# Kernel tuning notes

Measured on AMD Instinct MI355X. Metric: run time of the kernel, lower is better.

The kernel has to match this reference:

```python
import jax, jax.numpy as jnp
import numpy as np
from jax import lax

# --- STE quantizers matching the torch autograd.Functions ---
@jax.custom_vjp
def binary_quantize_w(x):
    return jnp.sign(x)

def _bqw_fwd(x):
    return jnp.sign(x), None

def _bqw_bwd(_, g):
    return (g,)  # straight-through identity

binary_quantize_w.defvjp(_bqw_fwd, _bqw_bwd)

@jax.custom_vjp
def binary_quantize_a(x):
    return jnp.sign(x)

def _bqa_fwd(x):
    return jnp.sign(x), x

def _bqa_bwd(x, g):
    return (jnp.clip(2.0 - jnp.abs(2.0 * x), a_min=0.0) * g,)

binary_quantize_a.defvjp(_bqa_fwd, _bqa_bwd)

STRIDE = 1
PAD = 1

def setup_inputs() -> dict:
    key = jax.random.key(0)
    k1, k2, k3 = jax.random.split(key, 3)
    x = jax.random.normal(k1, (32, 256, 56, 56), dtype=jnp.float32)
    M = jax.random.normal(k2, (256, 256, 3, 3), dtype=jnp.float32)
    Alpha = jax.random.uniform(k3, (256, 1, 1), dtype=jnp.float32)
    return {"x": x, "M": M, "Alpha": Alpha}

def reference(x, M, Alpha):
    bw = binary_quantize_w(M)        # (O, I, kh, kw), +/-1
    ba = binary_quantize_a(x)        # (N, C, H, W), +/-1
    out = lax.conv_general_dilated(
        ba, bw,
        window_strides=(STRIDE, STRIDE),
        padding=[(PAD, PAD), (PAD, PAD)],
        dimension_numbers=("NCHW", "OIHW", "NCHW"),
    )
    # Alpha (O,1,1) broadcasts over (N, O, H, W) trailing dims -> per-channel scale
    return out * Alpha
```

## Files before the change

### kernel.cpp

```cpp
#include <hip/hip_runtime.h>
#include <stdint.h>


typedef __attribute__((ext_vector_type(16))) float floatx16;
typedef __attribute__((ext_vector_type(8)))  int   intx8;

#define N_IMG 32
#define C_IN  256
#define O_OUT 256
#define HP 58
#define WP 58
#define GPI 3136
#define APAD_POS ((size_t)N_IMG * HP * WP)
#define APAD_BYTES (APAD_POS * C_IN)
#define TPI 13
#define AL_GRAN 1072
#define WL_GRAN 1536
#define WPK_STEP 49152

__device__ __forceinline__ unsigned int sgn8(float x) {
    return x > 0.f ? 0x38u : (x < 0.f ? 0xB8u : 0u);
}

__device__ __forceinline__ void glds16(const unsigned char* g, unsigned char* l) {
    __builtin_amdgcn_global_load_lds(
        (const __attribute__((address_space(1))) unsigned int*)g,
        (__attribute__((address_space(3))) unsigned int*)l, 16, 0, 0);
}

__global__ __launch_bounds__(256) void binarize_act(
    const float* __restrict__ x, unsigned char* __restrict__ apad)
{
    int bid = blockIdx.x;
    int n = bid / HP;
    int hp = bid - n * HP;
    int tid = threadIdx.x;

    unsigned char* rowp = apad + ((size_t)(n * HP + hp) * WP) * C_IN;
    uint4 z = {0u, 0u, 0u, 0u};

    if (hp == 0 || hp == HP - 1) {
#pragma unroll
        for (int j = 0; j < 4; ++j) {
            int t = tid + 256 * j;
            if (t < WP * 16) {
                int w = t >> 4, g = t & 15;
                *(uint4*)(rowp + (size_t)w * C_IN + g * 16) = z;
            }
        }
        return;
    }
    int h = hp - 1;

    __shared__ unsigned int tile[C_IN * 15];
    __shared__ unsigned int lds2[56 * 65];

    const float* xb = x + ((size_t)n * C_IN) * GPI + h * 56;
#pragma unroll
    for (int j = 0; j < 14; ++j) {
        int t = tid + 256 * j;
        int ci = t / 14;
        int w4 = t - ci * 14;
        float4 v = *(const float4*)(xb + (size_t)ci * GPI + w4 * 4);
        tile[ci * 15 + w4] = sgn8(v.x) | (sgn8(v.y) << 8) |
                             (sgn8(v.z) << 16) | (sgn8(v.w) << 24);
    }
    __syncthreads();

#pragma unroll
    for (int j = 0; j < 14; ++j) {
        int t = tid + 256 * j;
        int wlo = t & 3;
        int cq  = (t >> 2) & 63;
        int whi = t >> 8;
        int sh = wlo * 8;
        unsigned int r = 0;
#pragma unroll
        for (int i = 0; i < 4; ++i) {
            unsigned int v = tile[(cq * 4 + i) * 15 + whi];
            r |= ((v >> sh) & 0xFFu) << (8 * i);
        }
        lds2[(whi * 4 + wlo) * 65 + cq] = r;
    }
    __syncthreads();

#pragma unroll
    for (int j = 0; j < 4; ++j) {
        int t = tid + 256 * j;
        if (t < 896) {
            int w = t >> 4, g = t & 15;
            uint4 v;
            v.x = lds2[w * 65 + g * 4 + 0];
            v.y = lds2[w * 65 + g * 4 + 1];
            v.z = lds2[w * 65 + g * 4 + 2];
            v.w = lds2[w * 65 + g * 4 + 3];
            *(uint4*)(rowp + (size_t)(w + 1) * C_IN + g * 16) = v;
        }
    }
    if (tid < 32) {
        int g = tid & 15;
        int col = (tid >> 4) * (WP - 1);
        *(uint4*)(rowp + (size_t)col * C_IN + g * 16) = z;
    }
}

__global__ __launch_bounds__(64) void pack_w(
    const float* __restrict__ M, unsigned char* __restrict__ wpk)
{
    int gid = blockIdx.x * 64 + threadIdx.x;
    int o = gid >> 6;
    int c4 = (gid & 63) << 2;
    int c0q = c4 >> 6;
    int c63 = c4 & 63;
    const float* mb = M + (size_t)(o * C_IN + c4) * 9;
#pragma unroll
    for (int t = 0; t < 9; ++t) {
        int kh = t / 3, kw = t - 3 * (t / 3);
        unsigned int r = sgn8(mb[t]) | (sgn8(mb[9 + t]) << 8) |
                         (sgn8(mb[18 + t]) << 16) | (sgn8(mb[27 + t]) << 24);
        size_t dst = ((size_t)(kh * 4 + c0q) * 3 + kw) * 16384 + o * 64 + c63;
        *(unsigned int*)(wpk + dst) = r;
    }
}

__global__ __launch_bounds__(256, 2) void bconv_gemm(
    const unsigned char* __restrict__ apad,
    const unsigned char* __restrict__ wpk,
    const float* __restrict__ alpha,
    float* __restrict__ out)
{
    __shared__ __align__(16) unsigned char Al[AL_GRAN * 16];
    __shared__ __align__(16) unsigned char Wl[WL_GRAN * 16];

    const int tid = threadIdx.x;
    const int wv = tid >> 6, lane = tid & 63;
    const int l31 = lane & 31, hb = lane >> 5;

    const int hw = blockIdx.x;
    const int bid = (hw & 7) * 104 + (hw >> 3);

    const int img = bid / 26;
    const int rem = bid - img * 26;
    const int tl = rem >> 1, ot = rem & 1;
    const int g0 = tl << 8;
    const int h0 = g0 / 56, w0 = g0 - h0 * 56;
    const int o_base = ot << 7;
    const int Q0 = (img * HP + h0) * WP + w0;

    int al_pos[5], al_sl[5];
#pragma unroll
    for (int it = 0; it < 5; ++it) {
        int s = (it < 4) ? (tid + (it << 8)) : (tid + 816);
        int pos = s >> 2, gI = s & 3;
        al_pos[it] = pos;
        al_sl[it]  = ((gI ^ ((pos >> 1) & 3)) << 4);
    }
    int wl_src[6];
#pragma unroll
    for (int it = 0; it < 6; ++it) {
        int s = tid + (it << 8);
        int r = s >> 2, q = s & 3;
        int kw = r >> 7, ol = r & 127;
        wl_src[it] = kw * 16384 + (o_base + ol) * 64 + ((q ^ ((r >> 1) & 3)) << 4);
    }

    const int o_half  = (wv >> 1) << 6;
    const int px_half = (wv & 1) << 7;

    int pos_tab[4], pxg[4];
#pragma unroll
    for (int nt = 0; nt < 4; ++nt) {
        int px = px_half + (nt << 5) + l31;
        pxg[nt] = g0 + px;
        int pxc = (pxg[nt] < GPI) ? px : (GPI - 1 - g0);
        pos_tab[nt] = pxc + 2 * ((w0 + pxc) / 56);
    }

    floatx16 acc[2][4] = {};

    for (int t = 0; t < 12; ++t) {
        const int kh = t >> 2, c0 = (t & 3) << 6;
        const int rowbase = Q0 + kh * WP;
        const int plim = (int)APAD_POS - 1 - rowbase;
        const unsigned char* asrc = apad + (((size_t)rowbase << 8) + c0);
        const unsigned char* wsrc = wpk + (size_t)t * WPK_STEP;

        __syncthreads();
#pragma unroll
        for (int it = 0; it < 5; ++it) {
            int p = al_pos[it] < plim ? al_pos[it] : plim;
            int dst = (it < 4) ? ((it << 8) + (wv << 6)) : (816 + (wv << 6));
            glds16(asrc + ((size_t)p << 8) + al_sl[it], &Al[(size_t)dst << 4]);
        }
#pragma unroll
        for (int it = 0; it < 6; ++it)
            glds16(wsrc + wl_src[it], &Wl[(size_t)(tid + (it << 8)) << 4]);
        __syncthreads();

#pragma unroll
        for (int kw = 0; kw < 3; ++kw) {
            union F { uint4 q[2]; intx8 v; };
            F af[2];
#pragma unroll
            for (int mt = 0; mt < 2; ++mt) {
                int rl = (kw << 7) + o_half + (mt << 5) + l31;
                int m3 = (rl >> 1) & 3;
                af[mt].q[0] = *(const uint4*)&Wl[(size_t)(rl << 6) + ((((hb << 1))     ^ m3) << 4)];
                af[mt].q[1] = *(const uint4*)&Wl[(size_t)(rl << 6) + ((((hb << 1) | 1) ^ m3) << 4)];
            }
#pragma unroll
            for (int nt = 0; nt < 4; ++nt) {
                int pos = pos_tab[nt] + kw;
                int rb = pos << 6;
                int m3 = (pos >> 1) & 3;
                F bf;
                bf.q[0] = *(const uint4*)&Al[rb + ((((hb << 1))     ^ m3) << 4)];
                bf.q[1] = *(const uint4*)&Al[rb + ((((hb << 1) | 1) ^ m3) << 4)];
#pragma unroll
                for (int mt = 0; mt < 2; ++mt)
                    acc[mt][nt] = __builtin_amdgcn_mfma_scale_f32_32x32x64_f8f6f4(
                        af[mt].v, bf.v, acc[mt][nt],
                        0, 0,
                        0, 0x7F7F7F7F,
                        0, 0x7F7F7F7F);
            }
        }
    }

#pragma unroll
    for (int mt = 0; mt < 2; ++mt) {
#pragma unroll
        for (int r = 0; r < 16; ++r) {
            int o_loc = o_half + (mt << 5) + (r & 3) + ((r >> 2) << 3) + (hb << 2);
            int o_g = o_base + o_loc;
            float a = alpha[o_g];
            float* ob = out + ((size_t)(img * O_OUT + o_g)) * GPI;
#pragma unroll
            for (int nt = 0; nt < 4; ++nt) {
                if (pxg[nt] < GPI) ob[pxg[nt]] = acc[mt][nt][r] * a;
            }
        }
    }
}

extern "C" void kernel_launch(void* const* d_in, const int* in_sizes, int n_in,
                              void* d_out, int out_size, void* d_ws, size_t ws_size,
                              hipStream_t stream) {
    const float* x     = (const float*)d_in[0];
    const float* M     = (const float*)d_in[1];
    const float* alpha = (const float*)d_in[2];
    float* out = (float*)d_out;

    unsigned char* apad = (unsigned char*)d_ws;
    unsigned char* wpk  = apad + APAD_BYTES;

    binarize_act<<<dim3(N_IMG * HP), dim3(256), 0, stream>>>(x, apad);
    pack_w<<<dim3(256), dim3(64), 0, stream>>>(M, wpk);
    bconv_gemm<<<dim3(N_IMG * TPI * 2), dim3(256), 0, stream>>>(apad, wpk, alpha, out);
}
```

Before: 263.5 us.

## Switch binary conv operands from FP8 to FP4 packing in MFMA

Activations and weights are packed as FP4 (e2m1, ±1 encoded as nibbles) instead of FP8, which halves the padded activation and packed weight buffers. The LDS tiles, the global-to-LDS load counts and the fragment reads shrink to match, and the scaled MFMA is invoked with FP4 format codes. This is meant to cut global and LDS traffic and may raise MFMA throughput, in exchange for extra nibble-packing work in the binarize kernel and a new swizzle scheme.

```diff
diff --git a/kernel.cpp b/kernel.cpp
--- a/kernel.cpp
+++ b/kernel.cpp
@@ -12,20 +12,30 @@
 #define WP 58
 #define GPI 3136
 #define APAD_POS ((size_t)N_IMG * HP * WP)
-#define APAD_BYTES (APAD_POS * C_IN)
+#define ROWB 128
+#define APAD_BYTES (APAD_POS * ROWB)
 #define TPI 13
-#define AL_GRAN 1072
-#define WL_GRAN 1536
-#define WPK_STEP 49152
-
-__device__ __forceinline__ unsigned int sgn8(float x) {
-    return x > 0.f ? 0x38u : (x < 0.f ? 0xB8u : 0u);
+#define AL_CHUNKS 536
+#define WL_CHUNKS 768
+#define WROW 8192
+#define WPK_STEP (3 * WROW)
+
+__device__ __forceinline__ unsigned int sgn4(float x) {
+    return x > 0.f ? 0x2u : (x < 0.f ? 0xAu : 0u);
 }
 
 __device__ __forceinline__ void glds16(const unsigned char* g, unsigned char* l) {
     __builtin_amdgcn_global_load_lds(
         (const __attribute__((address_space(1))) unsigned int*)g,
         (__attribute__((address_space(3))) unsigned int*)l, 16, 0, 0);
+}
+
+__device__ __forceinline__ unsigned int nib16(unsigned int w) {
+    return (w & 0xFu) | ((w >> 4) & 0xF0u) |
+           ((w >> 8) & 0xF00u) | ((w >> 12) & 0xF000u);
+}
+__device__ __forceinline__ unsigned int nibc(unsigned int lo, unsigned int hi) {
+    return nib16(lo) | (nib16(hi) << 16);
 }
 
 __global__ __launch_bounds__(256) void binarize_act(
@@ -36,16 +46,16 @@
     int hp = bid - n * HP;
     int tid = threadIdx.x;
 
-    unsigned char* rowp = apad + ((size_t)(n * HP + hp) * WP) * C_IN;
+    unsigned char* rowp = apad + (size_t)(n * HP + hp) * WP * ROWB;
     uint4 z = {0u, 0u, 0u, 0u};
 
     if (hp == 0 || hp == HP - 1) {
 #pragma unroll
-        for (int j = 0; j < 4; ++j) {
+        for (int j = 0; j < 2; ++j) {
             int t = tid + 256 * j;
-            if (t < WP * 16) {
-                int w = t >> 4, g = t & 15;
-                *(uint4*)(rowp + (size_t)w * C_IN + g * 16) = z;
+            if (t < WP * 8) {
+                int w = t >> 3, g = t & 7;
+                *(uint4*)(rowp + (size_t)w * ROWB + g * 16) = z;
             }
         }
         return;
@@ -62,8 +72,8 @@
         int ci = t / 14;
         int w4 = t - ci * 14;
         float4 v = *(const float4*)(xb + (size_t)ci * GPI + w4 * 4);
-        tile[ci * 15 + w4] = sgn8(v.x) | (sgn8(v.y) << 8) |
-                             (sgn8(v.z) << 16) | (sgn8(v.w) << 24);
+        tile[ci * 15 + w4] = sgn4(v.x) | (sgn4(v.y) << 8) |
+                             (sgn4(v.z) << 16) | (sgn4(v.w) << 24);
     }
     __syncthreads();
 
@@ -85,22 +95,24 @@
     __syncthreads();
 
 #pragma unroll
-    for (int j = 0; j < 4; ++j) {
+    for (int j = 0; j < 2; ++j) {
         int t = tid + 256 * j;
-        if (t < 896) {
-            int w = t >> 4, g = t & 15;
+        if (t < 448) {
+            int w = t >> 3, g = t & 7;
+            uint4 a = *(uint4*)&lds2[w * 65 + g * 8];
+            uint4 b = *(uint4*)&lds2[w * 65 + g * 8 + 4];
             uint4 v;
-            v.x = lds2[w * 65 + g * 4 + 0];
-            v.y = lds2[w * 65 + g * 4 + 1];
-            v.z = lds2[w * 65 + g * 4 + 2];
-            v.w = lds2[w * 65 + g * 4 + 3];
-            *(uint4*)(rowp + (size_t)(w + 1) * C_IN + g * 16) = v;
-        }
-    }
-    if (tid < 32) {
-        int g = tid & 15;
-        int col = (tid >> 4) * (WP - 1);
-        *(uint4*)(rowp + (size_t)col * C_IN + g * 16) = z;
+            v.x = nibc(a.x, a.y);
+            v.y = nibc(a.z, a.w);
+            v.z = nibc(b.x, b.y);
+            v.w = nibc(b.z, b.w);
+            *(uint4*)(rowp + (size_t)(w + 1) * ROWB + g * 16) = v;
+        }
+    }
+    if (tid < 16) {
+        int g = tid & 7;
+        int col = (tid >> 3) * (WP - 1);
+        *(uint4*)(rowp + (size_t)col * ROWB + g * 16) = z;
     }
 }
 
@@ -111,15 +123,15 @@
     int o = gid >> 6;
     int c4 = (gid & 63) << 2;
     int c0q = c4 >> 6;
-    int c63 = c4 & 63;
+    int half = (c4 & 63) >> 1;
     const float* mb = M + (size_t)(o * C_IN + c4) * 9;
 #pragma unroll
     for (int t = 0; t < 9; ++t) {
         int kh = t / 3, kw = t - 3 * (t / 3);
-        unsigned int r = sgn8(mb[t]) | (sgn8(mb[9 + t]) << 8) |
-                         (sgn8(mb[18 + t]) << 16) | (sgn8(mb[27 + t]) << 24);
-        size_t dst = ((size_t)(kh * 4 + c0q) * 3 + kw) * 16384 + o * 64 + c63;
-        *(unsigned int*)(wpk + dst) = r;
+        unsigned int r = sgn4(mb[t]) | (sgn4(mb[9 + t]) << 4) |
+                         (sgn4(mb[18 + t]) << 8) | (sgn4(mb[27 + t]) << 12);
+        size_t dst = (size_t)((kh * 4 + c0q) * 3 + kw) * WROW + o * 32 + half;
+        *(unsigned short*)(wpk + dst) = (unsigned short)r;
     }
 }
 
@@ -129,8 +141,8 @@
     const float* __restrict__ alpha,
     float* __restrict__ out)
 {
-    __shared__ __align__(16) unsigned char Al[AL_GRAN * 16];
-    __shared__ __align__(16) unsigned char Wl[WL_GRAN * 16];
+    __shared__ __align__(16) unsigned char Al[AL_CHUNKS * 16];
+    __shared__ __align__(16) unsigned char Wl[WL_CHUNKS * 16];
 
     const int tid = threadIdx.x;
     const int wv = tid >> 6, lane = tid & 63;
@@ -147,21 +159,24 @@
     const int o_base = ot << 7;
     const int Q0 = (img * HP + h0) * WP + w0;
 
-    int al_pos[5], al_sl[5];
-#pragma unroll
-    for (int it = 0; it < 5; ++it) {
-        int s = (it < 4) ? (tid + (it << 8)) : (tid + 816);
-        int pos = s >> 2, gI = s & 3;
+    int al_pos[3], al_co[3], al_dst[3], al_on[3];
+#pragma unroll
+    for (int it = 0; it < 3; ++it) {
+        int g = (it < 2) ? (tid + (it << 8)) : (512 + tid);
+        al_on[it] = (it < 2) || (tid < AL_CHUNKS - 512);
+        int pos = g >> 1;
         al_pos[it] = pos;
-        al_sl[it]  = ((gI ^ ((pos >> 1) & 3)) << 4);
-    }
-    int wl_src[6];
-#pragma unroll
-    for (int it = 0; it < 6; ++it) {
-        int s = tid + (it << 8);
-        int r = s >> 2, q = s & 3;
+        al_co[it]  = (((g & 1) ^ ((pos >> 2) & 1)) << 4);
+        al_dst[it] = g << 4;
+    }
+    int wl_src[3], wl_dst[3];
+#pragma unroll
+    for (int it = 0; it < 3; ++it) {
+        int g = tid + (it << 8);
+        int r = g >> 1, q = (g & 1) ^ ((r >> 2) & 1);
         int kw = r >> 7, ol = r & 127;
-        wl_src[it] = kw * 16384 + (o_base + ol) * 64 + ((q ^ ((r >> 1) & 3)) << 4);
+        wl_src[it] = kw * WROW + (o_base + ol) * 32 + (q << 4);
+        wl_dst[it] = g << 4;
     }
 
     const int o_half  = (wv >> 1) << 6;
@@ -177,24 +192,27 @@
     }
 
     floatx16 acc[2][4] = {};
+    const uint4 z4 = {0u, 0u, 0u, 0u};
 
     for (int t = 0; t < 12; ++t) {
-        const int kh = t >> 2, c0 = (t & 3) << 6;
+        const int kh = t >> 2;
+        const int cb0 = (t & 3) << 5;
         const int rowbase = Q0 + kh * WP;
         const int plim = (int)APAD_POS - 1 - rowbase;
-        const unsigned char* asrc = apad + (((size_t)rowbase << 8) + c0);
+        const unsigned char* asrc = apad + ((size_t)rowbase * ROWB + cb0);
         const unsigned char* wsrc = wpk + (size_t)t * WPK_STEP;
 
         __syncthreads();
 #pragma unroll
-        for (int it = 0; it < 5; ++it) {
-            int p = al_pos[it] < plim ? al_pos[it] : plim;
-            int dst = (it < 4) ? ((it << 8) + (wv << 6)) : (816 + (wv << 6));
-            glds16(asrc + ((size_t)p << 8) + al_sl[it], &Al[(size_t)dst << 4]);
-        }
-#pragma unroll
-        for (int it = 0; it < 6; ++it)
-            glds16(wsrc + wl_src[it], &Wl[(size_t)(tid + (it << 8)) << 4]);
+        for (int it = 0; it < 3; ++it) {
+            if (al_on[it]) {
+                int p = al_pos[it] < plim ? al_pos[it] : plim;
+                glds16(asrc + (size_t)p * ROWB + al_co[it], &Al[al_dst[it]]);
+            }
+        }
+#pragma unroll
+        for (int it = 0; it < 3; ++it)
+            glds16(wsrc + wl_src[it], &Wl[wl_dst[it]]);
         __syncthreads();
 
 #pragma unroll
@@ -204,23 +222,22 @@
 #pragma unroll
             for (int mt = 0; mt < 2; ++mt) {
                 int rl = (kw << 7) + o_half + (mt << 5) + l31;
-                int m3 = (rl >> 1) & 3;
-                af[mt].q[0] = *(const uint4*)&Wl[(size_t)(rl << 6) + ((((hb << 1))     ^ m3) << 4)];
-                af[mt].q[1] = *(const uint4*)&Wl[(size_t)(rl << 6) + ((((hb << 1) | 1) ^ m3) << 4)];
+                int L = (rl << 1) + (hb ^ ((rl >> 2) & 1));
+                af[mt].q[0] = *(const uint4*)&Wl[(size_t)L << 4];
+                af[mt].q[1] = z4;
             }
 #pragma unroll
             for (int nt = 0; nt < 4; ++nt) {
                 int pos = pos_tab[nt] + kw;
-                int rb = pos << 6;
-                int m3 = (pos >> 1) & 3;
+                int L = (pos << 1) + (hb ^ ((pos >> 2) & 1));
                 F bf;
-                bf.q[0] = *(const uint4*)&Al[rb + ((((hb << 1))     ^ m3) << 4)];
-                bf.q[1] = *(const uint4*)&Al[rb + ((((hb << 1) | 1) ^ m3) << 4)];
+                bf.q[0] = *(const uint4*)&Al[(size_t)L << 4];
+                bf.q[1] = z4;
 #pragma unroll
                 for (int mt = 0; mt < 2; ++mt)
                     acc[mt][nt] = __builtin_amdgcn_mfma_scale_f32_32x32x64_f8f6f4(
                         af[mt].v, bf.v, acc[mt][nt],
-                        0, 0,
+                        4, 4,
                         0, 0x7F7F7F7F,
                         0, 0x7F7F7F7F);
             }
```

After: 243.2 us. 1.08x faster.
